# Kernel optimization log

Hardware: AMD Instinct MI355X
Metric: run time of the kernel (lower is better)

The kernel has to match this reference:

```python
import jax, jax.numpy as jnp
import numpy as np

B, N, DIM_IN, DIM, DIM_C, RES, PAD, NBLK = 4, 32768, 3, 128, 128, 64, 0.1, 5
R2 = RES * RES
PLANES = ((0, 2), (0, 1), (1, 2))  # xz, xy, yz as in ConvONet


def setup_inputs() -> dict:
    key = jax.random.key(0)
    ks = jax.random.split(key, 8)
    x = jax.random.uniform(ks[0], (B, N, DIM_IN), minval=-0.55, maxval=0.55, dtype=jnp.float32)
    w = lambda k, sh: (jax.random.normal(k, sh, dtype=jnp.float32) * 0.02)
    return {
        "x": x,
        "stem_w": w(ks[1], (DIM_IN, 2 * DIM)), "stem_b": jnp.zeros((2 * DIM,), jnp.float32),
        "blk_fc0_w": w(ks[2], (NBLK, 2 * DIM, DIM)), "blk_fc0_b": jnp.zeros((NBLK, DIM), jnp.float32),
        "blk_fc1_w": w(ks[3], (NBLK, DIM, DIM)), "blk_fc1_b": jnp.zeros((NBLK, DIM), jnp.float32),
        "blk_sc_w": w(ks[4], (NBLK, 2 * DIM, DIM)), "blk_sc_b": jnp.zeros((NBLK, DIM), jnp.float32),
        "fc_c_w": w(ks[5], (DIM, DIM_C)), "fc_c_b": jnp.zeros((DIM_C,), jnp.float32),
    }


def _tri_indices(xyz):
    # per-plane flat grid index, ConvONet-style normalization with padding
    idxs = []
    for (a, b) in PLANES:
        p = xyz[..., (a, b)] / (1.0 + PAD + 1e-3) + 0.5
        p = jnp.clip(p, 0.0, 1.0 - 1e-6)
        ij = jnp.clip((p * RES).astype(jnp.int32), 0, RES - 1)
        idxs.append(ij[..., 0] + RES * ij[..., 1])  # (B, N)
    return idxs


def _scatter(c, idx, reduction):
    # c: (B, N, D), idx: (B, N) -> (B, R2, D)
    b, n, d = c.shape
    seg = (idx + jnp.arange(b, dtype=idx.dtype)[:, None] * R2).reshape(-1)
    flat = c.reshape(b * n, d)
    if reduction == "max":
        out = jax.ops.segment_max(flat, seg, num_segments=b * R2)
        out = jnp.where(jnp.isfinite(out), out, jnp.zeros((), c.dtype))  # empty cells -> 0
    else:  # mean
        s = jax.ops.segment_sum(flat, seg, num_segments=b * R2)
        cnt = jax.ops.segment_sum(jnp.ones((b * n, 1), c.dtype), seg, num_segments=b * R2)
        out = s / jnp.maximum(cnt, 1.0)
    return out.reshape(b, R2, d)


def _pool_local(h, idxs):
    # scatter-max into each triplane, gather back per-point, sum over the 3 planes
    out = jnp.zeros_like(h)
    for idx in idxs:
        grid = _scatter(h, idx, "max")                       # (B, R2, D)
        out = out + jnp.take_along_axis(grid, idx[..., None], axis=1)
    return out


def _block(h, w0, b0, w1, b1, ws, bs):
    # pre-activation residual MLP (ResnetBlockFC)
    net = jax.nn.relu(h) @ w0 + b0
    dx = jax.nn.relu(net) @ w1 + b1
    return h @ ws + bs + dx


def reference(x, stem_w, stem_b, blk_fc0_w, blk_fc0_b, blk_fc1_w, blk_fc1_b,
              blk_sc_w, blk_sc_b, fc_c_w, fc_c_b):
    xyz = x[..., :3]
    idxs = _tri_indices(xyz)
    h = x @ stem_w + stem_b                                  # (B, N, 2*DIM)
    h = _block(h, blk_fc0_w[0], blk_fc0_b[0], blk_fc1_w[0], blk_fc1_b[0], blk_sc_w[0], blk_sc_b[0])
    for i in range(1, NBLK):
        h = jnp.concatenate([h, _pool_local(h, idxs)], axis=-1)
        h = _block(h, blk_fc0_w[i], blk_fc0_b[i], blk_fc1_w[i], blk_fc1_b[i], blk_sc_w[i], blk_sc_b[i])
    c = h @ fc_c_w + fc_c_b                                  # (B, N, DIM_C)
    tri = jnp.stack([_scatter(c, idx, "mean") for idx in idxs])  # (3, B, R2, DIM_C)
    # flat index = i + RES*j -> reshape gives (j, i); move channels to front
    tri = tri.reshape(3, B, RES, RES, DIM_C).transpose(0, 1, 4, 2, 3)  # (3, B, DIM_C, RES, RES)
    return (xyz, c, tri)
```

## Files before the change

### kernel.cpp

```cpp
#include <hip/hip_runtime.h>
#include <hip/hip_bf16.h>

#define B_   4
#define NPTS 32768
#define BN   131072
#define RES  64
#define R2   4096
#define DIM  128
#define K2   256
#define NBLK 5
#define NSEG (3*B_*R2)

typedef __bf16 bf16x8 __attribute__((ext_vector_type(8)));
typedef float  f32x16 __attribute__((ext_vector_type(16)));
typedef unsigned int uintv4 __attribute__((ext_vector_type(4)));

#define MFMA(a,b,c) __builtin_amdgcn_mfma_f32_32x32x16_bf16((a),(b),(c),0,0,0)

#define O_IDX  0
#define O_CNT  (O_IDX + 3*BN*4)
#define O_OFF  (O_CNT + NSEG*4)
#define O_WOFF (O_OFF + NSEG*4)
#define O_LIST (O_WOFF + NSEG*4)
#define O_H    (O_LIST + 3*BN*4)
#define O_GRID (O_H + BN*DIM*2)
#define O_W    (O_GRID + NSEG*DIM*2)
#define WBLK_ELEMS 81920

#define OUT_C_OFF   393216
#define OUT_TRI_OFF 17170432

__device__ __forceinline__ unsigned short f2bf(float f){
  unsigned int u = __float_as_uint(f);
  return (unsigned short)((u + 0x7fffu + ((u >> 16) & 1u)) >> 16);
}
__device__ __forceinline__ float bflo(unsigned int u){ return __uint_as_float(u << 16); }
__device__ __forceinline__ float bfhi(unsigned int u){ return __uint_as_float(u & 0xffff0000u); }
__device__ __forceinline__ int coord_bin(float u){
  float p = u / 1.101f + 0.5f;
  p = fminf(fmaxf(p, 0.0f), (float)(1.0 - 1e-6));
  int i = (int)(p * 64.0f);
  return i < 0 ? 0 : (i > 63 ? 63 : i);
}
__device__ __forceinline__ unsigned int pk_relu(unsigned int a){
  unsigned int r, z = 0;
  asm("v_pk_max_f16 %0, %1, %2" : "=v"(r) : "v"(a), "v"(z));
  return r;
}
__device__ __forceinline__ bf16x8 relu8(bf16x8 v){
  uintv4 u = __builtin_bit_cast(uintv4, v);
  u[0] = pk_relu(u[0]); u[1] = pk_relu(u[1]); u[2] = pk_relu(u[2]); u[3] = pk_relu(u[3]);
  return __builtin_bit_cast(bf16x8, u);
}

__global__ void k_prep(const float* __restrict__ x, float* __restrict__ out_xyz,
                       int* __restrict__ idx, int* __restrict__ cnt){
  int p = blockIdx.x * 256 + threadIdx.x;
  if (p >= BN) return;
  float x0 = x[p*3+0], x1 = x[p*3+1], x2 = x[p*3+2];
  out_xyz[p*3+0] = x0; out_xyz[p*3+1] = x1; out_xyz[p*3+2] = x2;
  int b = p >> 15;
  int c0 = coord_bin(x0) + 64*coord_bin(x2);
  int c1 = coord_bin(x0) + 64*coord_bin(x1);
  int c2 = coord_bin(x1) + 64*coord_bin(x2);
  idx[0*BN+p] = c0; idx[1*BN+p] = c1; idx[2*BN+p] = c2;
  atomicAdd(&cnt[(0*B_+b)*R2 + c0], 1);
  atomicAdd(&cnt[(1*B_+b)*R2 + c1], 1);
  atomicAdd(&cnt[(2*B_+b)*R2 + c2], 1);
}

__global__ __launch_bounds__(1024) void k_scan(const int* __restrict__ cnt,
                                               int* __restrict__ off, int* __restrict__ woff){
  __shared__ int part[1024];
  const int t = threadIdx.x;
  const int PER = NSEG / 1024;
  const int base = t * PER;
  int s = 0;
  for (int i = 0; i < PER; ++i) s += cnt[base+i];
  part[t] = s;
  __syncthreads();
  for (int d = 1; d < 1024; d <<= 1){
    int v = (t >= d) ? part[t-d] : 0;
    __syncthreads();
    part[t] += v;
    __syncthreads();
  }
  int acc = (t == 0) ? 0 : part[t-1];
  for (int i = 0; i < PER; ++i){
    int c = cnt[base+i];
    off[base+i] = acc; woff[base+i] = acc;
    acc += c;
  }
}

__global__ void k_bin(const int* __restrict__ idx, int* __restrict__ woff, int* __restrict__ list){
  int p = blockIdx.x * 256 + threadIdx.x;
  if (p >= BN) return;
  int b = p >> 15;
  #pragma unroll
  for (int pl = 0; pl < 3; ++pl){
    int cell = idx[pl*BN + p];
    int s = (pl*B_+b)*R2 + cell;
    int slot = atomicAdd(&woff[s], 1);
    list[slot] = p;
  }
}

__global__ void k_prepw(const float* __restrict__ fc0, const float* __restrict__ fc1,
                        const float* __restrict__ scw, const float* __restrict__ fcc,
                        unsigned short* __restrict__ wdst){
  int t = blockIdx.x * 256 + threadIdx.x;
  if (t < 163840){
    int b = t >> 15, r = t & 32767;
    int j = r & 7, l = (r >> 3) & 63, ks = (r >> 9) & 15, w = r >> 13;
    int n = w*32 + (l & 31);
    int k = ks*16 + (l >> 5)*8 + j;
    wdst[b*WBLK_ELEMS + r] = f2bf(fc0[(b*256 + k)*128 + n]);
  } else if (t < 327680){
    int t2 = t - 163840;
    int b = t2 >> 15, r = t2 & 32767;
    int j = r & 7, l = (r >> 3) & 63, ks = (r >> 9) & 15, w = r >> 13;
    int n = w*32 + (l & 31);
    int k = ks*16 + (l >> 5)*8 + j;
    wdst[b*WBLK_ELEMS + 32768 + r] = f2bf(scw[(b*256 + k)*128 + n]);
  } else if (t < 409600){
    int t2 = t - 327680;
    int b = t2 >> 14, r = t2 & 16383;
    int j = r & 7, l = (r >> 3) & 63, ks = (r >> 9) & 7, w = (r >> 12) & 3;
    int n = w*32 + (l & 31);
    int k = ks*16 + (l >> 5)*8 + j;
    wdst[b*WBLK_ELEMS + 65536 + r] = f2bf(fc1[(b*128 + k)*128 + n]);
  } else if (t < 425984){
    int r = t - 409600;
    int j = r & 7, l = (r >> 3) & 63, ks = (r >> 9) & 7, w = (r >> 12) & 3;
    int n = w*32 + (l & 31);
    int k = ks*16 + (l >> 5)*8 + j;
    wdst[5*WBLK_ELEMS + r] = f2bf(fcc[k*128 + n]);
  }
}

__global__ __launch_bounds__(256) void k_cellmax(const unsigned short* __restrict__ h,
    const int* __restrict__ off, const int* __restrict__ cnt,
    const int* __restrict__ list, unsigned short* __restrict__ gbf){
  const int seg = (blockIdx.x * 256 + threadIdx.x) >> 6;
  const int l = threadIdx.x & 63;
  const int base = off[seg], n = cnt[seg];
  float m0 = -INFINITY, m1 = -INFINITY;
  int i = 0;
  for (; i + 4 <= n; i += 4){
    int p0 = list[base+i], p1 = list[base+i+1], p2 = list[base+i+2], p3 = list[base+i+3];
    unsigned int u0 = *(const unsigned int*)(h + p0*DIM + 2*l);
    unsigned int u1 = *(const unsigned int*)(h + p1*DIM + 2*l);
    unsigned int u2 = *(const unsigned int*)(h + p2*DIM + 2*l);
    unsigned int u3 = *(const unsigned int*)(h + p3*DIM + 2*l);
    m0 = fmaxf(fmaxf(fmaxf(m0, bflo(u0)), fmaxf(bflo(u1), bflo(u2))), bflo(u3));
    m1 = fmaxf(fmaxf(fmaxf(m1, bfhi(u0)), fmaxf(bfhi(u1), bfhi(u2))), bfhi(u3));
  }
  for (; i < n; ++i){
    int p = list[base+i];
    unsigned int u = *(const unsigned int*)(h + p*DIM + 2*l);
    m0 = fmaxf(m0, bflo(u)); m1 = fmaxf(m1, bfhi(u));
  }
  unsigned int o = 0;
  if (n > 0) o = (__float_as_uint(m0) >> 16) | (__float_as_uint(m1) & 0xffff0000u);
  *(unsigned int*)(gbf + (size_t)seg*DIM + 2*l) = o;
}

template<int MODE>
__global__ __launch_bounds__(256, 4) void k_block(
    const float* __restrict__ x,
    const float* __restrict__ stem_w, const float* __restrict__ stem_b,
    unsigned short* __restrict__ h,
    const unsigned short* __restrict__ gbf, const int* __restrict__ idx,
    const unsigned short* __restrict__ wT,
    const float* __restrict__ b0g, const float* __restrict__ b1g, const float* __restrict__ bsg)
{
  __shared__ unsigned short lh2[64*256];
  const int t = threadIdx.x;
  const int tile0 = blockIdx.x * 64;

  if (MODE == 0){
    const int dg8 = (t & 31) * 8;
    const int prow = t >> 5;
    float wa[8], wb[8], wc[8], bb[8];
    #pragma unroll
    for (int j = 0; j < 8; ++j){
      wa[j] = stem_w[dg8+j]; wb[j] = stem_w[256+dg8+j]; wc[j] = stem_w[512+dg8+j];
      bb[j] = stem_b[dg8+j];
    }
    #pragma unroll 4
    for (int pass = 0; pass < 8; ++pass){
      int p = prow + pass*8;
      int pg = tile0 + p;
      float x0 = x[pg*3+0], x1 = x[pg*3+1], x2 = x[pg*3+2];
      unsigned int pk[4];
      #pragma unroll
      for (int j = 0; j < 4; ++j){
        float v0 = bb[2*j]   + x0*wa[2*j]   + x1*wb[2*j]   + x2*wc[2*j];
        float v1 = bb[2*j+1] + x0*wa[2*j+1] + x1*wb[2*j+1] + x2*wc[2*j+1];
        pk[j] = (unsigned int)f2bf(v0) | ((unsigned int)f2bf(v1) << 16);
      }
      uint4 q; q.x = pk[0]; q.y = pk[1]; q.z = pk[2]; q.w = pk[3];
      *(uint4*)((char*)lh2 + p*512 + ((dg8*2) ^ ((p & 7) << 4))) = q;
    }
  } else {
    const int dg4 = (t & 31) * 4;
    const int prow = t >> 5;
    #pragma unroll 4
    for (int pass = 0; pass < 8; ++pass){
      int p = prow + pass*8;
      int pg = tile0 + p;
      int b = pg >> 15;
      uint2 hv = *(const uint2*)(h + pg*DIM + dg4);
      *(uint2*)((char*)lh2 + p*512 + ((dg4*2) ^ ((p & 7) << 4))) = hv;
      float s0 = 0.f, s1 = 0.f, s2 = 0.f, s3 = 0.f;
      #pragma unroll
      for (int pl = 0; pl < 3; ++pl){
        int cell = idx[pl*BN + pg];
        const unsigned short* g = gbf + ((size_t)((pl*B_+b)*R2 + cell))*DIM + dg4;
        uint2 gv = *(const uint2*)g;
        s0 += bflo(gv.x); s1 += bfhi(gv.x); s2 += bflo(gv.y); s3 += bfhi(gv.y);
      }
      uint2 pv;
      pv.x = (unsigned int)f2bf(s0) | ((unsigned int)f2bf(s1) << 16);
      pv.y = (unsigned int)f2bf(s2) | ((unsigned int)f2bf(s3) << 16);
      *(uint2*)((char*)lh2 + p*512 + (((128 + dg4)*2) ^ ((p & 7) << 4))) = pv;
    }
  }
  __syncthreads();

  const int w  = t >> 6;
  const int l  = t & 63;
  const int lm = l & 31;
  const int hi = l >> 5;
  const int D0 = w * 32;
  const int swz  = (lm & 7) << 4;
  const unsigned short* w0f = wT +          ((size_t)w*16*64 + l)*8;
  const unsigned short* wsf = wT + 32768 +  ((size_t)w*16*64 + l)*8;
  const unsigned short* w1f = wT + 65536 +  ((size_t)w* 8*64 + l)*8;

  f32x16 an0, an1, as0, as1;
  #pragma unroll
  for (int i = 0; i < 16; ++i){ an0[i] = 0.f; an1[i] = 0.f; as0[i] = 0.f; as1[i] = 0.f; }

  const char* lr0 = (const char*)lh2 + lm*512;
  const char* lr1 = (const char*)lh2 + (32+lm)*512;

  #pragma unroll 4
  for (int ks = 0; ks < 16; ++ks){
    bf16x8 a0 = *(const bf16x8*)(w0f + ks*512);
    bf16x8 a1 = *(const bf16x8*)(wsf + ks*512);
    int kb = (ks*32 + hi*16) ^ swz;
    bf16x8 br0 = *(const bf16x8*)(lr0 + kb);
    bf16x8 br1 = *(const bf16x8*)(lr1 + kb);
    an0 = MFMA(a0, relu8(br0), an0);
    as0 = MFMA(a1, br0, as0);
    an1 = MFMA(a0, relu8(br1), an1);
    as1 = MFMA(a1, br1, as1);
  }

  __syncthreads();

  {
    char* nr0 = (char*)lh2 + lm*256;
    char* nr1 = (char*)lh2 + (32+lm)*256;
    #pragma unroll
    for (int g = 0; g < 4; ++g){
      int d0 = D0 + 8*g + 4*hi;
      float q0 = b0g[d0], q1 = b0g[d0+1], q2 = b0g[d0+2], q3 = b0g[d0+3];
      uint2 u0, u1;
      {
        float v0 = fmaxf(an0[4*g+0]+q0, 0.f), v1 = fmaxf(an0[4*g+1]+q1, 0.f);
        float v2 = fmaxf(an0[4*g+2]+q2, 0.f), v3 = fmaxf(an0[4*g+3]+q3, 0.f);
        u0.x = (unsigned int)f2bf(v0) | ((unsigned int)f2bf(v1) << 16);
        u0.y = (unsigned int)f2bf(v2) | ((unsigned int)f2bf(v3) << 16);
      }
      {
        float v0 = fmaxf(an1[4*g+0]+q0, 0.f), v1 = fmaxf(an1[4*g+1]+q1, 0.f);
        float v2 = fmaxf(an1[4*g+2]+q2, 0.f), v3 = fmaxf(an1[4*g+3]+q3, 0.f);
        u1.x = (unsigned int)f2bf(v0) | ((unsigned int)f2bf(v1) << 16);
        u1.y = (unsigned int)f2bf(v2) | ((unsigned int)f2bf(v3) << 16);
      }
      int ob = (d0*2) ^ swz;
      *(uint2*)(nr0 + ob) = u0;
      *(uint2*)(nr1 + ob) = u1;
    }
  }
  __syncthreads();

  f32x16 ad0, ad1;
  #pragma unroll
  for (int i = 0; i < 16; ++i){ ad0[i] = 0.f; ad1[i] = 0.f; }
  const char* nr0c = (const char*)lh2 + lm*256;
  const char* nr1c = (const char*)lh2 + (32+lm)*256;
  #pragma unroll 4
  for (int ks = 0; ks < 8; ++ks){
    bf16x8 a = *(const bf16x8*)(w1f + ks*512);
    int kb = (ks*32 + hi*16) ^ swz;
    ad0 = MFMA(a, *(const bf16x8*)(nr0c + kb), ad0);
    ad1 = MFMA(a, *(const bf16x8*)(nr1c + kb), ad1);
  }

  #pragma unroll
  for (int g = 0; g < 4; ++g){
    int d0 = D0 + 8*g + 4*hi;
    float p0 = b1g[d0]   + bsg[d0];
    float p1 = b1g[d0+1] + bsg[d0+1];
    float p2 = b1g[d0+2] + bsg[d0+2];
    float p3 = b1g[d0+3] + bsg[d0+3];
    {
      int pg = tile0 + lm;
      float v0 = as0[4*g+0]+ad0[4*g+0]+p0, v1 = as0[4*g+1]+ad0[4*g+1]+p1;
      float v2 = as0[4*g+2]+ad0[4*g+2]+p2, v3 = as0[4*g+3]+ad0[4*g+3]+p3;
      uint2 o;
      o.x = (unsigned int)f2bf(v0) | ((unsigned int)f2bf(v1) << 16);
      o.y = (unsigned int)f2bf(v2) | ((unsigned int)f2bf(v3) << 16);
      *(uint2*)(h + pg*DIM + d0) = o;
    }
    {
      int pg = tile0 + 32 + lm;
      float v0 = as1[4*g+0]+ad1[4*g+0]+p0, v1 = as1[4*g+1]+ad1[4*g+1]+p1;
      float v2 = as1[4*g+2]+ad1[4*g+2]+p2, v3 = as1[4*g+3]+ad1[4*g+3]+p3;
      uint2 o;
      o.x = (unsigned int)f2bf(v0) | ((unsigned int)f2bf(v1) << 16);
      o.y = (unsigned int)f2bf(v2) | ((unsigned int)f2bf(v3) << 16);
      *(uint2*)(h + pg*DIM + d0) = o;
    }
  }
}

__global__ __launch_bounds__(256) void k_final(
    const unsigned short* __restrict__ h,
    const unsigned short* __restrict__ fcf, const float* __restrict__ fcb,
    float* __restrict__ cout)
{
  __shared__ unsigned short lh[64*128];
  const int t = threadIdx.x;
  const int tile0 = blockIdx.x * 64;
  {
    int dg4 = (t & 31) * 4, prow = t >> 5;
    #pragma unroll 4
    for (int pass = 0; pass < 8; ++pass){
      int p = prow + pass*8, pg = tile0 + p;
      uint2 hv = *(const uint2*)(h + pg*DIM + dg4);
      *(uint2*)((char*)lh + p*256 + ((dg4*2) ^ ((p & 7) << 4))) = hv;
    }
  }
  __syncthreads();
  const int w = t >> 6, l = t & 63, lm = l & 31, hi = l >> 5;
  const int D0 = w*32, swz = (lm & 7) << 4;
  const unsigned short* fw = fcf + ((size_t)w*8*64 + l)*8;
  f32x16 ac0, ac1;
  #pragma unroll
  for (int i = 0; i < 16; ++i){ ac0[i] = 0.f; ac1[i] = 0.f; }
  const char* r0 = (const char*)lh + lm*256;
  const char* r1 = (const char*)lh + (32+lm)*256;
  #pragma unroll 4
  for (int ks = 0; ks < 8; ++ks){
    bf16x8 a = *(const bf16x8*)(fw + ks*512);
    int kb = (ks*32 + hi*16) ^ swz;
    ac0 = MFMA(a, *(const bf16x8*)(r0 + kb), ac0);
    ac1 = MFMA(a, *(const bf16x8*)(r1 + kb), ac1);
  }
  #pragma unroll
  for (int g = 0; g < 4; ++g){
    int d0 = D0 + 8*g + 4*hi;
    float q0 = fcb[d0], q1 = fcb[d0+1], q2 = fcb[d0+2], q3 = fcb[d0+3];
    {
      int pg = tile0 + lm;
      float4 f4;
      f4.x = ac0[4*g+0]+q0; f4.y = ac0[4*g+1]+q1; f4.z = ac0[4*g+2]+q2; f4.w = ac0[4*g+3]+q3;
      *(float4*)(cout + (size_t)pg*DIM + d0) = f4;
    }
    {
      int pg = tile0 + 32 + lm;
      float4 f4;
      f4.x = ac1[4*g+0]+q0; f4.y = ac1[4*g+1]+q1; f4.z = ac1[4*g+2]+q2; f4.w = ac1[4*g+3]+q3;
      *(float4*)(cout + (size_t)pg*DIM + d0) = f4;
    }
  }
}

__global__ __launch_bounds__(256) void k_trisum(const float* __restrict__ c,
    const int* __restrict__ off, const int* __restrict__ cnt,
    const int* __restrict__ list, float* __restrict__ tri){
  __shared__ float ls[64*130];
  const int t = threadIdx.x;
  const int wg = blockIdx.x;
  const int pl = wg >> 8;
  const int b  = (wg >> 6) & 3;
  const int r  = wg & 63;
  const int segbase = (pl*B_+b)*R2 + r*64;
  const int wv = t >> 6, l = t & 63;
  for (int cc = wv*16; cc < wv*16+16; ++cc){
    int s = segbase + cc;
    int base = off[s], n = cnt[s];
    float s0 = 0.f, s1 = 0.f;
    int i = 0;
    for (; i + 2 <= n; i += 2){
      int p0 = list[base+i], p1 = list[base+i+1];
      float2 v0 = *(const float2*)(c + (size_t)p0*DIM + 2*l);
      float2 v1 = *(const float2*)(c + (size_t)p1*DIM + 2*l);
      s0 += v0.x + v1.x; s1 += v0.y + v1.y;
    }
    if (i < n){
      int p = list[base+i];
      float2 v = *(const float2*)(c + (size_t)p*DIM + 2*l);
      s0 += v.x; s1 += v.y;
    }
    float den = (float)(n < 1 ? 1 : n);
    ls[cc*130 + 2*l]   = s0 / den;
    ls[cc*130 + 2*l+1] = s1 / den;
  }
  __syncthreads();
  float* dst = tri + (size_t)((pl*B_+b)*DIM) * R2 + r*64;
  for (int i = 0; i < 32; ++i){
    int li = t + i*256;
    int d = li >> 6, cc = li & 63;
    dst[(size_t)d*R2 + cc] = ls[cc*130 + d];
  }
}

extern "C" void kernel_launch(void* const* d_in, const int* in_sizes, int n_in,
                              void* d_out, int out_size, void* d_ws, size_t ws_size,
                              hipStream_t stream){
  const float* x      = (const float*)d_in[0];
  const float* stem_w = (const float*)d_in[1];
  const float* stem_b = (const float*)d_in[2];
  const float* fc0_w  = (const float*)d_in[3];
  const float* fc0_b  = (const float*)d_in[4];
  const float* fc1_w  = (const float*)d_in[5];
  const float* fc1_b  = (const float*)d_in[6];
  const float* sc_w   = (const float*)d_in[7];
  const float* sc_b   = (const float*)d_in[8];
  const float* fcc_w  = (const float*)d_in[9];
  const float* fcc_b  = (const float*)d_in[10];

  char* ws = (char*)d_ws;
  int* idx            = (int*)(ws + O_IDX);
  int* cnt            = (int*)(ws + O_CNT);
  int* off            = (int*)(ws + O_OFF);
  int* woff           = (int*)(ws + O_WOFF);
  int* list           = (int*)(ws + O_LIST);
  unsigned short* h   = (unsigned short*)(ws + O_H);
  unsigned short* gbf = (unsigned short*)(ws + O_GRID);
  unsigned short* wbf = (unsigned short*)(ws + O_W);

  float* out     = (float*)d_out;
  float* out_xyz = out;
  float* out_c   = out + OUT_C_OFF;
  float* out_tri = out + OUT_TRI_OFF;

  hipMemsetAsync(cnt, 0, NSEG*4, stream);
  k_prep<<<BN/256, 256, 0, stream>>>(x, out_xyz, idx, cnt);
  k_prepw<<<1664, 256, 0, stream>>>(fc0_w, fc1_w, sc_w, fcc_w, wbf);
  k_scan<<<1, 1024, 0, stream>>>(cnt, off, woff);
  k_bin<<<BN/256, 256, 0, stream>>>(idx, woff, list);

  k_block<0><<<BN/64, 256, 0, stream>>>(x, stem_w, stem_b, h, nullptr, nullptr,
                                        wbf, fc0_b, fc1_b, sc_b);
  for (int i = 1; i < NBLK; ++i){
    k_cellmax<<<NSEG/4, 256, 0, stream>>>(h, off, cnt, list, gbf);
    k_block<1><<<BN/64, 256, 0, stream>>>(nullptr, nullptr, nullptr, h, gbf, idx,
                                          wbf + (size_t)i*WBLK_ELEMS,
                                          fc0_b + i*DIM, fc1_b + i*DIM, sc_b + i*DIM);
  }
  k_final<<<BN/64, 256, 0, stream>>>(h, wbf + (size_t)5*WBLK_ELEMS, fcc_b, out_c);
  k_trisum<<<768, 256, 0, stream>>>(out_c, off, cnt, list, out_tri);
}
```

Measured before the change: 447.2 us.

## Interleave plane indices, split triplane mean into cellsum and transpose kernels

Per-point plane cell indices move from three separate arrays to one interleaved int4 array, so k_bin and k_block load them with a single vector load; k_block now prefetches all eight index vectors and issues the three grid loads together. The final triplane mean, previously done by 768 workgroups each handling 64 cells serially per wave, is split into a k_cellsum kernel with one wave per cell (unrolled by 4) writing into a scratch grid, followed by a separate k_tritr transpose kernel. The goal is more parallelism and memory-level concurrency in the gather-reduce. The cost is an extra launch and an extra round trip of the summed grid through memory. The scratch grid reuses the h buffer, which is safe only because h is dead after k_final.

```diff
diff --git a/kernel.cpp b/kernel.cpp
--- a/kernel.cpp
+++ b/kernel.cpp
@@ -18,7 +18,7 @@
 #define MFMA(a,b,c) __builtin_amdgcn_mfma_f32_32x32x16_bf16((a),(b),(c),0,0,0)
 
 #define O_IDX  0
-#define O_CNT  (O_IDX + 3*BN*4)
+#define O_CNT  (O_IDX + BN*16)
 #define O_OFF  (O_CNT + NSEG*4)
 #define O_WOFF (O_OFF + NSEG*4)
 #define O_LIST (O_WOFF + NSEG*4)
@@ -54,7 +54,7 @@
 }
 
 __global__ void k_prep(const float* __restrict__ x, float* __restrict__ out_xyz,
-                       int* __restrict__ idx, int* __restrict__ cnt){
+                       int* __restrict__ idx4, int* __restrict__ cnt){
   int p = blockIdx.x * 256 + threadIdx.x;
   if (p >= BN) return;
   float x0 = x[p*3+0], x1 = x[p*3+1], x2 = x[p*3+2];
@@ -63,7 +63,8 @@
   int c0 = coord_bin(x0) + 64*coord_bin(x2);
   int c1 = coord_bin(x0) + 64*coord_bin(x1);
   int c2 = coord_bin(x1) + 64*coord_bin(x2);
-  idx[0*BN+p] = c0; idx[1*BN+p] = c1; idx[2*BN+p] = c2;
+  int4 c4; c4.x = c0; c4.y = c1; c4.z = c2; c4.w = 0;
+  *(int4*)(idx4 + p*4) = c4;
   atomicAdd(&cnt[(0*B_+b)*R2 + c0], 1);
   atomicAdd(&cnt[(1*B_+b)*R2 + c1], 1);
   atomicAdd(&cnt[(2*B_+b)*R2 + c2], 1);
@@ -93,14 +94,15 @@
   }
 }
 
-__global__ void k_bin(const int* __restrict__ idx, int* __restrict__ woff, int* __restrict__ list){
+__global__ void k_bin(const int* __restrict__ idx4, int* __restrict__ woff, int* __restrict__ list){
   int p = blockIdx.x * 256 + threadIdx.x;
   if (p >= BN) return;
   int b = p >> 15;
+  int4 c4 = *(const int4*)(idx4 + p*4);
+  int cs[3] = {c4.x, c4.y, c4.z};
   #pragma unroll
   for (int pl = 0; pl < 3; ++pl){
-    int cell = idx[pl*BN + p];
-    int s = (pl*B_+b)*R2 + cell;
+    int s = (pl*B_+b)*R2 + cs[pl];
     int slot = atomicAdd(&woff[s], 1);
     list[slot] = p;
   }
@@ -171,7 +173,7 @@
     const float* __restrict__ x,
     const float* __restrict__ stem_w, const float* __restrict__ stem_b,
     unsigned short* __restrict__ h,
-    const unsigned short* __restrict__ gbf, const int* __restrict__ idx,
+    const unsigned short* __restrict__ gbf, const int* __restrict__ idx4,
     const unsigned short* __restrict__ wT,
     const float* __restrict__ b0g, const float* __restrict__ b1g, const float* __restrict__ bsg)
 {
@@ -206,21 +208,27 @@
   } else {
     const int dg4 = (t & 31) * 4;
     const int prow = t >> 5;
+    int4 cl[8];
+    #pragma unroll
+    for (int pass = 0; pass < 8; ++pass)
+      cl[pass] = *(const int4*)(idx4 + (tile0 + prow + pass*8)*4);
     #pragma unroll 4
     for (int pass = 0; pass < 8; ++pass){
       int p = prow + pass*8;
       int pg = tile0 + p;
       int b = pg >> 15;
       uint2 hv = *(const uint2*)(h + pg*DIM + dg4);
+      const unsigned short* g0 = gbf + ((size_t)((0*B_+b)*R2 + cl[pass].x))*DIM + dg4;
+      const unsigned short* g1 = gbf + ((size_t)((1*B_+b)*R2 + cl[pass].y))*DIM + dg4;
+      const unsigned short* g2 = gbf + ((size_t)((2*B_+b)*R2 + cl[pass].z))*DIM + dg4;
+      uint2 v0 = *(const uint2*)g0;
+      uint2 v1 = *(const uint2*)g1;
+      uint2 v2 = *(const uint2*)g2;
       *(uint2*)((char*)lh2 + p*512 + ((dg4*2) ^ ((p & 7) << 4))) = hv;
-      float s0 = 0.f, s1 = 0.f, s2 = 0.f, s3 = 0.f;
-      #pragma unroll
-      for (int pl = 0; pl < 3; ++pl){
-        int cell = idx[pl*BN + pg];
-        const unsigned short* g = gbf + ((size_t)((pl*B_+b)*R2 + cell))*DIM + dg4;
-        uint2 gv = *(const uint2*)g;
-        s0 += bflo(gv.x); s1 += bfhi(gv.x); s2 += bflo(gv.y); s3 += bfhi(gv.y);
-      }
+      float s0 = bflo(v0.x) + bflo(v1.x) + bflo(v2.x);
+      float s1 = bfhi(v0.x) + bfhi(v1.x) + bfhi(v2.x);
+      float s2 = bflo(v0.y) + bflo(v1.y) + bflo(v2.y);
+      float s3 = bfhi(v0.y) + bfhi(v1.y) + bfhi(v2.y);
       uint2 pv;
       pv.x = (unsigned int)f2bf(s0) | ((unsigned int)f2bf(s1) << 16);
       pv.y = (unsigned int)f2bf(s2) | ((unsigned int)f2bf(s3) << 16);
@@ -381,43 +389,57 @@
   }
 }
 
-__global__ __launch_bounds__(256) void k_trisum(const float* __restrict__ c,
+__global__ __launch_bounds__(256) void k_cellsum(const float* __restrict__ c,
     const int* __restrict__ off, const int* __restrict__ cnt,
-    const int* __restrict__ list, float* __restrict__ tri){
-  __shared__ float ls[64*130];
+    const int* __restrict__ list, float* __restrict__ sgrid){
+  const int seg = (blockIdx.x * 256 + threadIdx.x) >> 6;
+  const int l = threadIdx.x & 63;
+  const int base = off[seg], n = cnt[seg];
+  float s0 = 0.f, s1 = 0.f;
+  int i = 0;
+  for (; i + 4 <= n; i += 4){
+    int p0 = list[base+i], p1 = list[base+i+1], p2 = list[base+i+2], p3 = list[base+i+3];
+    float2 v0 = *(const float2*)(c + (size_t)p0*DIM + 2*l);
+    float2 v1 = *(const float2*)(c + (size_t)p1*DIM + 2*l);
+    float2 v2 = *(const float2*)(c + (size_t)p2*DIM + 2*l);
+    float2 v3 = *(const float2*)(c + (size_t)p3*DIM + 2*l);
+    s0 += (v0.x + v1.x) + (v2.x + v3.x);
+    s1 += (v0.y + v1.y) + (v2.y + v3.y);
+  }
+  for (; i < n; ++i){
+    int p = list[base+i];
+    float2 v = *(const float2*)(c + (size_t)p*DIM + 2*l);
+    s0 += v.x; s1 += v.y;
+  }
+  float den = 1.0f / (float)(n < 1 ? 1 : n);
+  float2 o; o.x = s0 * den; o.y = s1 * den;
+  *(float2*)(sgrid + (size_t)seg*DIM + 2*l) = o;
+}
+
+__global__ __launch_bounds__(256) void k_tritr(const float* __restrict__ sgrid,
+                                               float* __restrict__ tri){
+  __shared__ float ls[64*129];
   const int t = threadIdx.x;
   const int wg = blockIdx.x;
   const int pl = wg >> 8;
   const int b  = (wg >> 6) & 3;
   const int r  = wg & 63;
   const int segbase = (pl*B_+b)*R2 + r*64;
-  const int wv = t >> 6, l = t & 63;
-  for (int cc = wv*16; cc < wv*16+16; ++cc){
-    int s = segbase + cc;
-    int base = off[s], n = cnt[s];
-    float s0 = 0.f, s1 = 0.f;
-    int i = 0;
-    for (; i + 2 <= n; i += 2){
-      int p0 = list[base+i], p1 = list[base+i+1];
-      float2 v0 = *(const float2*)(c + (size_t)p0*DIM + 2*l);
-      float2 v1 = *(const float2*)(c + (size_t)p1*DIM + 2*l);
-      s0 += v0.x + v1.x; s1 += v0.y + v1.y;
-    }
-    if (i < n){
-      int p = list[base+i];
-      float2 v = *(const float2*)(c + (size_t)p*DIM + 2*l);
-      s0 += v.x; s1 += v.y;
-    }
-    float den = (float)(n < 1 ? 1 : n);
-    ls[cc*130 + 2*l]   = s0 / den;
-    ls[cc*130 + 2*l+1] = s1 / den;
+  #pragma unroll 4
+  for (int i = 0; i < 16; ++i){
+    int f = t + i*256;
+    int cell = f >> 6, d2 = f & 63;
+    float2 v = *(const float2*)(sgrid + (size_t)(segbase+cell)*DIM + d2*2);
+    ls[cell*129 + d2*2]   = v.x;
+    ls[cell*129 + d2*2+1] = v.y;
   }
   __syncthreads();
   float* dst = tri + (size_t)((pl*B_+b)*DIM) * R2 + r*64;
+  #pragma unroll 4
   for (int i = 0; i < 32; ++i){
     int li = t + i*256;
     int d = li >> 6, cc = li & 63;
-    dst[(size_t)d*R2 + cc] = ls[cc*130 + d];
+    dst[(size_t)d*R2 + cc] = ls[cc*129 + d];
   }
 }
 
@@ -437,12 +459,13 @@
   const float* fcc_b  = (const float*)d_in[10];
 
   char* ws = (char*)d_ws;
-  int* idx            = (int*)(ws + O_IDX);
+  int* idx4           = (int*)(ws + O_IDX);
   int* cnt            = (int*)(ws + O_CNT);
   int* off            = (int*)(ws + O_OFF);
   int* woff           = (int*)(ws + O_WOFF);
   int* list           = (int*)(ws + O_LIST);
   unsigned short* h   = (unsigned short*)(ws + O_H);
+  float* sgrid        = (float*)(ws + O_H);
   unsigned short* gbf = (unsigned short*)(ws + O_GRID);
   unsigned short* wbf = (unsigned short*)(ws + O_W);
 
@@ -452,19 +475,20 @@
   float* out_tri = out + OUT_TRI_OFF;
 
   hipMemsetAsync(cnt, 0, NSEG*4, stream);
-  k_prep<<<BN/256, 256, 0, stream>>>(x, out_xyz, idx, cnt);
+  k_prep<<<BN/256, 256, 0, stream>>>(x, out_xyz, idx4, cnt);
   k_prepw<<<1664, 256, 0, stream>>>(fc0_w, fc1_w, sc_w, fcc_w, wbf);
   k_scan<<<1, 1024, 0, stream>>>(cnt, off, woff);
-  k_bin<<<BN/256, 256, 0, stream>>>(idx, woff, list);
+  k_bin<<<BN/256, 256, 0, stream>>>(idx4, woff, list);
 
   k_block<0><<<BN/64, 256, 0, stream>>>(x, stem_w, stem_b, h, nullptr, nullptr,
                                         wbf, fc0_b, fc1_b, sc_b);
   for (int i = 1; i < NBLK; ++i){
     k_cellmax<<<NSEG/4, 256, 0, stream>>>(h, off, cnt, list, gbf);
-    k_block<1><<<BN/64, 256, 0, stream>>>(nullptr, nullptr, nullptr, h, gbf, idx,
+    k_block<1><<<BN/64, 256, 0, stream>>>(nullptr, nullptr, nullptr, h, gbf, idx4,
                                           wbf + (size_t)i*WBLK_ELEMS,
                                           fc0_b + i*DIM, fc1_b + i*DIM, sc_b + i*DIM);
   }
   k_final<<<BN/64, 256, 0, stream>>>(h, wbf + (size_t)5*WBLK_ELEMS, fcc_b, out_c);
-  k_trisum<<<768, 256, 0, stream>>>(out_c, off, cnt, list, out_tri);
-}
+  k_cellsum<<<NSEG/4, 256, 0, stream>>>(out_c, off, cnt, list, sgrid);
+  k_tritr<<<768, 256, 0, stream>>>(sgrid, out_tri);
+}
```

Result: slower. 479.3 us (+7.2%).
